# Kernel tuning notes

Measured on AMD Instinct MI355X. Metric: run time of the kernel, lower is better.

The kernel has to match this reference:

```python
import jax, jax.numpy as jnp
import numpy as np

N = 65536          # collocation points
NB = 32            # n_buses
H = 256            # hidden width (two hidden layers)
TMAX = 20.0        # t_max for input normalisation


def _glorot(k, shape):
    lim = np.sqrt(2.0 / (shape[0] + shape[1])).astype(np.float32)
    return jax.random.normal(k, shape, jnp.float32) * lim


def setup_inputs() -> dict:
    key = jax.random.key(0)
    ks = jax.random.split(key, 8)
    return {
        "input_time": jax.random.uniform(ks[0], (N, 1), jnp.float32) * TMAX,
        "input_power": jax.random.normal(ks[1], (N, NB), jnp.float32),
        "W0": _glorot(ks[2], (1, H)),   "b0": jnp.zeros((H,), jnp.float32),
        "W1": _glorot(ks[3], (H, H)),   "b1": jnp.zeros((H,), jnp.float32),
        "W2": _glorot(ks[4], (H, NB)),  "b2": jnp.zeros((NB,), jnp.float32),
        "lambda_m": jnp.ones((1, NB), jnp.float32),
        "lambda_d": jnp.ones((1, NB), jnp.float32),
        "lambda_b": jax.random.uniform(ks[5], (NB, NB), jnp.float32),
        "bus_with_inertia": jnp.ones((1, NB), jnp.float32),
    }


def reference(input_time, input_power, W0, b0, W1, b1, W2, b2,
              lambda_m, lambda_d, lambda_b, bus_with_inertia):
    def mlp(t):  # scalar time -> [NB] angles
        x = 2.0 * t / TMAX - 1.0          # NormaliseInputLayer (t_min = 0)
        h = jnp.tanh(x * W0[0] + b0)      # [H]
        h = jnp.tanh(h @ W1 + b1)         # [H]
        return h @ W2 + b2                # [NB]

    one = jnp.float32(1.0)

    def f_and_dt(t):
        return jax.jvp(mlp, (t,), (one,))  # (delta, d delta/dt)

    def all3(t):
        (out, out_t), (_, out_tt) = jax.jvp(f_and_dt, (t,), (one,))
        return out, out_t, out_tt

    # vectorize the nested forward-mode derivatives over all samples at once
    out, out_t, out_tt = jax.vmap(all3)(input_time[:, 0])  # each [N, NB]

    # pairwise sin coupling: sum_j B_ij * sin(delta_i - delta_j)
    diff = out[:, :, None] - out[:, None, :]               # [N, NB, NB]
    connectivity = jnp.sum(lambda_b * jnp.sin(diff), axis=2)  # [N, NB]

    physics = (lambda_m * bus_with_inertia * out_tt
               + lambda_d * out_t
               + connectivity - input_power)

    return out, out_t, physics
```

## Files before the change

### kernel.cpp

```cpp
#include <hip/hip_runtime.h>

#define NPTS 65536
#define NB 32
#define H 256

typedef __attribute__((ext_vector_type(8))) short bhalf8;
typedef __attribute__((ext_vector_type(4))) float f32x4;

union BHU { bhalf8 h; uint u[4]; };

__device__ __forceinline__ float bf2f(ushort u) {
  union { uint x; float f; } c; c.x = ((uint)u) << 16; return c.f;
}
__device__ __forceinline__ ushort f2bf(float f) {
  uint x = __float_as_uint(f);
  uint r = x + 0x7FFFu + ((x >> 16) & 1u);
  return (ushort)(r >> 16);
}
__device__ __forceinline__ uint packtr(float a, float b) {
  return (__float_as_uint(a) >> 16) | (__float_as_uint(b) & 0xFFFF0000u);
}
__device__ __forceinline__ float fast_tanh(float z) {
  float e = __expf(2.0f * z);
  return 1.0f - 2.0f / (e + 1.0f);
}

__device__ __forceinline__ bool detect_bf16(const void* W1) {
  const uint4* p = (const uint4*)W1;
  int cnt = 0;
#pragma unroll
  for (int i = 0; i < 8; i++) {
    uint4 v = p[i];
    uint d[4] = {v.x, v.y, v.z, v.w};
#pragma unroll
    for (int k = 0; k < 4; k++) {
      int e = (d[k] >> 7) & 0xFF;
      cnt += (e >= 0x70 && e <= 0x7E) ? 1 : 0;
    }
  }
  return cnt >= 16;
}

template<bool B16> __device__ __forceinline__ float LD(const void* p, int i) {
  if constexpr (B16) return bf2f(((const ushort*)p)[i]);
  else               return ((const float*)p)[i];
}
template<bool B16> __device__ __forceinline__ void ST(void* p, int i, float v) {
  if constexpr (B16) ((ushort*)p)[i] = f2bf(v);
  else               ((float*)p)[i] = v;
}

__global__ void swz_kernel(const void* W1, const void* W2,
                           ushort* __restrict__ W1s, ushort* __restrict__ W2s) {
  int gid = blockIdx.x * 256 + threadIdx.x;
  bool b16 = detect_bf16(W1);
  if (gid < 65536) {
    int r = gid & 15, q = (gid >> 4) & 3, j = (gid >> 6) & 7;
    int kk = (gid >> 9) & 7, ct = gid >> 12;
    int src = (kk * 32 + q * 8 + j) * H + ct * 16 + r;
    int dst = ((ct * 8 + kk) * 64 + q * 16 + r) * 8 + j;
    float v = b16 ? bf2f(((const ushort*)W1)[src]) : ((const float*)W1)[src];
    W1s[dst] = f2bf(v);
  } else {
    int g2 = gid - 65536;
    int r = g2 & 15, q = (g2 >> 4) & 3, j = (g2 >> 6) & 7;
    int kk = (g2 >> 9) & 7, ct = (g2 >> 12) & 1;
    int src = (kk * 32 + q * 8 + j) * NB + ct * 16 + r;
    int dst = ((ct * 8 + kk) * 64 + q * 16 + r) * 8 + j;
    float v = b16 ? bf2f(((const ushort*)W2)[src]) : ((const float*)W2)[src];
    W2s[dst] = f2bf(v);
  }
}

#define PPITCH 36
#define SPITCH 40

struct Smem {
  alignas(16) float  pair[4][48 * PPITCH];
  alignas(16) ushort scb[4][2 * 16 * SPITCH];
  alignas(16) ushort W2l[16 * 64 * 8];
  alignas(16) ushort lamTf[2 * 64 * 8];
  alignas(16) float  w0c[H], b0c[H], b1c[H];
  alignas(16) float  b2c[NB], lamMc[NB], lamDc[NB];
};

template<bool B16>
__device__ void pinn_body(Smem& sm,
                          const void* timeP, const void* powerP,
                          const void* W0, const void* b0,
                          const void* b1, const void* b2,
                          const void* lam_m, const void* lam_d,
                          const void* lam_b, const void* bwi,
                          const ushort* __restrict__ W1s, void* outP) {
  const int tid = threadIdx.x;
  const int wave = tid >> 6, lane = tid & 63;
  const int q = lane >> 4, r = lane & 15;

#pragma unroll
  for (int i = 0; i < 4; i++) {
    int c = tid + i * 256;
    *(bhalf8*)(sm.W2l + c * 8) = *(const bhalf8*)(((const ushort*)W1s) + H * H + c * 8);
  }
  if (tid < 128) {
    int ct = tid >> 6, l2 = tid & 63, qq = l2 >> 4, rr = l2 & 15;
    BHU t;
#pragma unroll
    for (int j = 0; j < 8; j += 2)
      t.u[j >> 1] = packtr(LD<B16>(lam_b, (ct * 16 + rr) * NB + qq * 8 + j),
                           LD<B16>(lam_b, (ct * 16 + rr) * NB + qq * 8 + j + 1));
    *(bhalf8*)(sm.lamTf + tid * 8) = t.h;
  }
  if (tid < H) {
    sm.w0c[tid] = LD<B16>(W0, tid);
    sm.b0c[tid] = LD<B16>(b0, tid);
    sm.b1c[tid] = LD<B16>(b1, tid);
  }
  if (tid < NB) {
    sm.b2c[tid]   = LD<B16>(b2, tid);
    sm.lamMc[tid] = LD<B16>(lam_m, tid) * LD<B16>(bwi, tid);
    sm.lamDc[tid] = LD<B16>(lam_d, tid);
  }
  __syncthreads();

  const int s0 = (blockIdx.x * 4 + wave) * 16;
  float* pb = &sm.pair[wave][0];
  ushort* sc = &sm.scb[wave][0];

  float t = LD<B16>(timeP, s0 + r);
  float x = t * 0.1f - 1.0f;

  bhalf8 a0f[8], a1f[8], a2f[8];
#pragma unroll
  for (int kk = 0; kk < 8; kk++) {
    int k0 = kk * 32 + q * 8;
    BHU t0, t1, t2;
    float vv[8], d1v[8], d2v[8];
#pragma unroll
    for (int j = 0; j < 8; j++) {
      float w0v = sm.w0c[k0 + j];
      float pre = x * w0v + sm.b0c[k0 + j];
      float v = fast_tanh(pre);
      float cc = w0v * 0.1f;
      float s2 = 1.0f - v * v;
      vv[j] = v; d1v[j] = s2 * cc; d2v[j] = -2.0f * v * d1v[j] * cc;
    }
#pragma unroll
    for (int j = 0; j < 8; j += 2) {
      t0.u[j >> 1] = packtr(vv[j], vv[j + 1]);
      t1.u[j >> 1] = packtr(d1v[j], d1v[j + 1]);
      t2.u[j >> 1] = packtr(d2v[j], d2v[j + 1]);
    }
    a0f[kk] = t0.h; a1f[kk] = t1.h; a2f[kk] = t2.h;
  }

  f32x4 acc2[3][2];
#pragma unroll
  for (int ch = 0; ch < 3; ch++)
#pragma unroll
    for (int c2 = 0; c2 < 2; c2++) { f32x4 z = {0.f,0.f,0.f,0.f}; acc2[ch][c2] = z; }

  bhalf8 bf[8];
#pragma unroll
  for (int kk = 0; kk < 8; kk++)
    bf[kk] = *(const bhalf8*)(W1s + ((0 * 8 + kk) * 64 + lane) * 8);

#pragma unroll 2
  for (int ct = 0; ct < 16; ct++) {
    bhalf8 bn[8];
    int ctn = (ct < 15) ? ct + 1 : 15;
#pragma unroll
    for (int kk = 0; kk < 8; kk++)
      bn[kk] = *(const bhalf8*)(W1s + ((ctn * 8 + kk) * 64 + lane) * 8);

    f32x4 c0 = {0.f,0.f,0.f,0.f}, c1 = c0, c2 = c0;
#pragma unroll
    for (int kk = 0; kk < 8; kk++) {
      c0 = __builtin_amdgcn_mfma_f32_16x16x32_bf16(a0f[kk], bf[kk], c0, 0, 0, 0);
      c1 = __builtin_amdgcn_mfma_f32_16x16x32_bf16(a1f[kk], bf[kk], c1, 0, 0, 0);
      c2 = __builtin_amdgcn_mfma_f32_16x16x32_bf16(a2f[kk], bf[kk], c2, 0, 0, 0);
    }
    float b1v = sm.b1c[ct * 16 + r];
    int lc = (ct & 1) * 16 + r;
#pragma unroll
    for (int i = 0; i < 4; i++) {
      float hv  = fast_tanh(c0[i] + b1v);
      float s2  = 1.0f - hv * hv;
      float hd  = s2 * c1[i];
      float hdd = s2 * c2[i] - 2.0f * hv * hd * c1[i];
      int row = q * 4 + i;
      pb[row * PPITCH + lc]              = hv;
      pb[(16 + row) * PPITCH + lc]       = hd;
      pb[(32 + row) * PPITCH + lc]       = hdd;
    }
    if (ct & 1) {
      int p = ct >> 1;
#pragma unroll
      for (int ch = 0; ch < 3; ch++) {
        const float4* rp = (const float4*)&pb[(ch * 16 + r) * PPITCH + q * 8];
        float4 u0 = rp[0], u1 = rp[1];
        BHU hf;
        hf.u[0] = packtr(u0.x, u0.y); hf.u[1] = packtr(u0.z, u0.w);
        hf.u[2] = packtr(u1.x, u1.y); hf.u[3] = packtr(u1.z, u1.w);
#pragma unroll
        for (int c2i = 0; c2i < 2; c2i++) {
          bhalf8 w2f = *(const bhalf8*)(sm.W2l + ((c2i * 8 + p) * 64 + lane) * 8);
          acc2[ch][c2i] = __builtin_amdgcn_mfma_f32_16x16x32_bf16(hf.h, w2f, acc2[ch][c2i], 0, 0, 0);
        }
      }
    }
#pragma unroll
    for (int kk = 0; kk < 8; kk++) bf[kk] = bn[kk];
  }

  float dv[2][4], dt[2][4], dtt[2][4], sn[2][4], cs[2][4], Pv[2][4];
#pragma unroll
  for (int c2 = 0; c2 < 2; c2++) {
    int b = c2 * 16 + r;
    float b2v = sm.b2c[b];
#pragma unroll
    for (int i = 0; i < 4; i++) {
      int n = s0 + q * 4 + i;
      Pv[c2][i] = LD<B16>(powerP, n * NB + b);
      dv[c2][i]  = acc2[0][c2][i] + b2v;
      dt[c2][i]  = acc2[1][c2][i];
      dtt[c2][i] = acc2[2][c2][i];
      sn[c2][i] = __sinf(dv[c2][i]);
      cs[c2][i] = __cosf(dv[c2][i]);
      sc[0 * 16 * SPITCH + (q * 4 + i) * SPITCH + b] = f2bf(sn[c2][i]);
      sc[1 * 16 * SPITCH + (q * 4 + i) * SPITCH + b] = f2bf(cs[c2][i]);
      ST<B16>(outP, n * NB + b, dv[c2][i]);
      ST<B16>(outP, NPTS * NB + n * NB + b, dt[c2][i]);
    }
  }
  bhalf8 snA = *(const bhalf8*)(sc + 0 * 16 * SPITCH + r * SPITCH + q * 8);
  bhalf8 csA = *(const bhalf8*)(sc + 1 * 16 * SPITCH + r * SPITCH + q * 8);
  f32x4 accC[2], accS[2];
#pragma unroll
  for (int c2 = 0; c2 < 2; c2++) {
    bhalf8 lt = *(const bhalf8*)(sm.lamTf + (c2 * 64 + lane) * 8);
    f32x4 z = {0.f,0.f,0.f,0.f};
    accC[c2] = __builtin_amdgcn_mfma_f32_16x16x32_bf16(csA, lt, z, 0, 0, 0);
    accS[c2] = __builtin_amdgcn_mfma_f32_16x16x32_bf16(snA, lt, z, 0, 0, 0);
  }
#pragma unroll
  for (int c2 = 0; c2 < 2; c2++) {
    int b = c2 * 16 + r;
    float lm = sm.lamMc[b], ld = sm.lamDc[b];
#pragma unroll
    for (int i = 0; i < 4; i++) {
      float conn = sn[c2][i] * accC[c2][i] - cs[c2][i] * accS[c2][i];
      float phys = lm * dtt[c2][i] + ld * dt[c2][i] + conn - Pv[c2][i];
      int n = s0 + q * 4 + i;
      ST<B16>(outP, 2 * NPTS * NB + n * NB + b, phys);
    }
  }
}

__global__ __launch_bounds__(256, 2)
void pinn_kernel(const void* timeP, const void* powerP,
                 const void* W0, const void* b0,
                 const void* b1, const void* b2,
                 const void* lam_m, const void* lam_d,
                 const void* lam_b, const void* bwi,
                 const void* W1_for_detect,
                 const ushort* __restrict__ W1s, void* outP) {
  __shared__ Smem sm;
  if (detect_bf16(W1_for_detect))
    pinn_body<true>(sm, timeP, powerP, W0, b0, b1, b2, lam_m, lam_d, lam_b, bwi,
                    W1s, outP);
  else
    pinn_body<false>(sm, timeP, powerP, W0, b0, b1, b2, lam_m, lam_d, lam_b, bwi,
                     W1s, outP);
}

extern "C" void kernel_launch(void* const* d_in, const int* in_sizes, int n_in,
                              void* d_out, int out_size, void* d_ws, size_t ws_size,
                              hipStream_t stream) {
  const void* timeP  = d_in[0];
  const void* powerP = d_in[1];
  const void* W0     = d_in[2];
  const void* b0     = d_in[3];
  const void* W1     = d_in[4];
  const void* b1     = d_in[5];
  const void* W2     = d_in[6];
  const void* b2     = d_in[7];
  const void* lam_m  = d_in[8];
  const void* lam_d  = d_in[9];
  const void* lam_b  = d_in[10];
  const void* bwi    = d_in[11];

  ushort* W1s = (ushort*)d_ws;
  ushort* W2s = W1s + H * H;

  swz_kernel<<<288, 256, 0, stream>>>(W1, W2, W1s, W2s);
  pinn_kernel<<<1024, 256, 0, stream>>>(timeP, powerP, W0, b0, b1, b2,
                                        lam_m, lam_d, lam_b, bwi, W1,
                                        W1s, d_out);
  (void)W2s;
}
```

Measured before the change: 128.4 us.

## Stage hidden activations as bf16, defer layer-2 MFMA, drop W1 prefetch, raise occupancy

After: 222.0 us. 1.73x slower.

```diff
diff --git a/kernel.cpp b/kernel.cpp
--- a/kernel.cpp
+++ b/kernel.cpp
@@ -17,8 +17,8 @@
   uint r = x + 0x7FFFu + ((x >> 16) & 1u);
   return (ushort)(r >> 16);
 }
-__device__ __forceinline__ uint packtr(float a, float b) {
-  return (__float_as_uint(a) >> 16) | (__float_as_uint(b) & 0xFFFF0000u);
+__device__ __forceinline__ uint packrne(float a, float b) {
+  return (uint)f2bf(a) | ((uint)f2bf(b) << 16);
 }
 __device__ __forceinline__ float fast_tanh(float z) {
   float e = __expf(2.0f * z);
@@ -72,12 +72,10 @@
   }
 }
 
-#define PPITCH 36
-#define SPITCH 40
+#define PPITCH 40
 
 struct Smem {
-  alignas(16) float  pair[4][48 * PPITCH];
-  alignas(16) ushort scb[4][2 * 16 * SPITCH];
+  alignas(16) ushort pairw[4][48 * PPITCH];
   alignas(16) ushort W2l[16 * 64 * 8];
   alignas(16) ushort lamTf[2 * 64 * 8];
   alignas(16) float  w0c[H], b0c[H], b1c[H];
@@ -106,8 +104,8 @@
     BHU t;
 #pragma unroll
     for (int j = 0; j < 8; j += 2)
-      t.u[j >> 1] = packtr(LD<B16>(lam_b, (ct * 16 + rr) * NB + qq * 8 + j),
-                           LD<B16>(lam_b, (ct * 16 + rr) * NB + qq * 8 + j + 1));
+      t.u[j >> 1] = packrne(LD<B16>(lam_b, (ct * 16 + rr) * NB + qq * 8 + j),
+                            LD<B16>(lam_b, (ct * 16 + rr) * NB + qq * 8 + j + 1));
     *(bhalf8*)(sm.lamTf + tid * 8) = t.h;
   }
   if (tid < H) {
@@ -123,8 +121,7 @@
   __syncthreads();
 
   const int s0 = (blockIdx.x * 4 + wave) * 16;
-  float* pb = &sm.pair[wave][0];
-  ushort* sc = &sm.scb[wave][0];
+  ushort* pw = &sm.pairw[wave][0];
 
   float t = LD<B16>(timeP, s0 + r);
   float x = t * 0.1f - 1.0f;
@@ -146,9 +143,9 @@
     }
 #pragma unroll
     for (int j = 0; j < 8; j += 2) {
-      t0.u[j >> 1] = packtr(vv[j], vv[j + 1]);
-      t1.u[j >> 1] = packtr(d1v[j], d1v[j + 1]);
-      t2.u[j >> 1] = packtr(d2v[j], d2v[j + 1]);
+      t0.u[j >> 1] = packrne(vv[j], vv[j + 1]);
+      t1.u[j >> 1] = packrne(d1v[j], d1v[j + 1]);
+      t2.u[j >> 1] = packrne(d2v[j], d2v[j + 1]);
     }
     a0f[kk] = t0.h; a1f[kk] = t1.h; a2f[kk] = t2.h;
   }
@@ -159,18 +156,25 @@
 #pragma unroll
     for (int c2 = 0; c2 < 2; c2++) { f32x4 z = {0.f,0.f,0.f,0.f}; acc2[ch][c2] = z; }
 
-  bhalf8 bf[8];
-#pragma unroll
-  for (int kk = 0; kk < 8; kk++)
-    bf[kk] = *(const bhalf8*)(W1s + ((0 * 8 + kk) * 64 + lane) * 8);
-
-#pragma unroll 2
+#pragma unroll 1
   for (int ct = 0; ct < 16; ct++) {
-    bhalf8 bn[8];
-    int ctn = (ct < 15) ? ct + 1 : 15;
+    bhalf8 bf[8];
 #pragma unroll
     for (int kk = 0; kk < 8; kk++)
-      bn[kk] = *(const bhalf8*)(W1s + ((ctn * 8 + kk) * 64 + lane) * 8);
+      bf[kk] = *(const bhalf8*)(W1s + ((ct * 8 + kk) * 64 + lane) * 8);
+
+    if (ct >= 2 && (ct & 1) == 0) {
+      int p = (ct >> 1) - 1;
+#pragma unroll
+      for (int ch = 0; ch < 3; ch++) {
+        bhalf8 hf = *(const bhalf8*)(pw + (ch * 16 + r) * PPITCH + q * 8);
+#pragma unroll
+        for (int c2i = 0; c2i < 2; c2i++) {
+          bhalf8 w2f = *(const bhalf8*)(sm.W2l + ((c2i * 8 + p) * 64 + lane) * 8);
+          acc2[ch][c2i] = __builtin_amdgcn_mfma_f32_16x16x32_bf16(hf, w2f, acc2[ch][c2i], 0, 0, 0);
+        }
+      }
+    }
 
     f32x4 c0 = {0.f,0.f,0.f,0.f}, c1 = c0, c2 = c0;
 #pragma unroll
@@ -188,28 +192,21 @@
       float hd  = s2 * c1[i];
       float hdd = s2 * c2[i] - 2.0f * hv * hd * c1[i];
       int row = q * 4 + i;
-      pb[row * PPITCH + lc]              = hv;
-      pb[(16 + row) * PPITCH + lc]       = hd;
-      pb[(32 + row) * PPITCH + lc]       = hdd;
-    }
-    if (ct & 1) {
-      int p = ct >> 1;
-#pragma unroll
-      for (int ch = 0; ch < 3; ch++) {
-        const float4* rp = (const float4*)&pb[(ch * 16 + r) * PPITCH + q * 8];
-        float4 u0 = rp[0], u1 = rp[1];
-        BHU hf;
-        hf.u[0] = packtr(u0.x, u0.y); hf.u[1] = packtr(u0.z, u0.w);
-        hf.u[2] = packtr(u1.x, u1.y); hf.u[3] = packtr(u1.z, u1.w);
-#pragma unroll
-        for (int c2i = 0; c2i < 2; c2i++) {
-          bhalf8 w2f = *(const bhalf8*)(sm.W2l + ((c2i * 8 + p) * 64 + lane) * 8);
-          acc2[ch][c2i] = __builtin_amdgcn_mfma_f32_16x16x32_bf16(hf.h, w2f, acc2[ch][c2i], 0, 0, 0);
-        }
+      pw[row * PPITCH + lc]        = f2bf(hv);
+      pw[(16 + row) * PPITCH + lc] = f2bf(hd);
+      pw[(32 + row) * PPITCH + lc] = f2bf(hdd);
+    }
+  }
+  {
+#pragma unroll
+    for (int ch = 0; ch < 3; ch++) {
+      bhalf8 hf = *(const bhalf8*)(pw + (ch * 16 + r) * PPITCH + q * 8);
+#pragma unroll
+      for (int c2i = 0; c2i < 2; c2i++) {
+        bhalf8 w2f = *(const bhalf8*)(sm.W2l + ((c2i * 8 + 7) * 64 + lane) * 8);
+        acc2[ch][c2i] = __builtin_amdgcn_mfma_f32_16x16x32_bf16(hf, w2f, acc2[ch][c2i], 0, 0, 0);
       }
     }
-#pragma unroll
-    for (int kk = 0; kk < 8; kk++) bf[kk] = bn[kk];
   }
 
   float dv[2][4], dt[2][4], dtt[2][4], sn[2][4], cs[2][4], Pv[2][4];
@@ -226,14 +223,14 @@
       dtt[c2][i] = acc2[2][c2][i];
       sn[c2][i] = __sinf(dv[c2][i]);
       cs[c2][i] = __cosf(dv[c2][i]);
-      sc[0 * 16 * SPITCH + (q * 4 + i) * SPITCH + b] = f2bf(sn[c2][i]);
-      sc[1 * 16 * SPITCH + (q * 4 + i) * SPITCH + b] = f2bf(cs[c2][i]);
+      pw[(q * 4 + i) * PPITCH + b]        = f2bf(sn[c2][i]);
+      pw[(16 + q * 4 + i) * PPITCH + b]   = f2bf(cs[c2][i]);
       ST<B16>(outP, n * NB + b, dv[c2][i]);
       ST<B16>(outP, NPTS * NB + n * NB + b, dt[c2][i]);
     }
   }
-  bhalf8 snA = *(const bhalf8*)(sc + 0 * 16 * SPITCH + r * SPITCH + q * 8);
-  bhalf8 csA = *(const bhalf8*)(sc + 1 * 16 * SPITCH + r * SPITCH + q * 8);
+  bhalf8 snA = *(const bhalf8*)(pw + r * PPITCH + q * 8);
+  bhalf8 csA = *(const bhalf8*)(pw + (16 + r) * PPITCH + q * 8);
   f32x4 accC[2], accS[2];
 #pragma unroll
   for (int c2 = 0; c2 < 2; c2++) {
@@ -256,7 +253,7 @@
   }
 }
 
-__global__ __launch_bounds__(256, 2)
+__global__ __launch_bounds__(256, 4)
 void pinn_kernel(const void* timeP, const void* powerP,
                  const void* W0, const void* b0,
                  const void* b1, const void* b2,
```
